# Kernel tuning notes

Hardware: AMD Instinct MI355X
Metric: run time of the kernel (lower is better)

## Reference

```python
import jax, jax.numpy as jnp
import numpy as np

B, C, H, W, A = 16, 4, 256, 256, 6
EPS = 1e-5


def _bn(z, s, b):
    # train-mode BatchNorm with batch size 1: reduce over (H, W) per channel, biased var
    m = z.mean((1, 2), keepdims=True)
    v = ((z - m) ** 2).mean((1, 2), keepdims=True)
    return (z - m) * jax.lax.rsqrt(v + EPS) * s[:, None, None] + b[:, None, None]


def _conv(z, w, pad, dil=1):
    # z: [C_in, H, W], w: [C_out, C_in, kh, kw]
    return jax.lax.conv_general_dilated(
        z[None], w, (1, 1), [(pad, pad), (pad, pad)],
        rhs_dilation=(dil, dil), dimension_numbers=("NCHW", "OIHW", "NCHW"))[0]


def _up2_axis(z, axis):
    # bilinear x2 with align_corners=True along one axis
    n = z.shape[axis]
    m = 2 * n
    pos = jnp.arange(m, dtype=jnp.float32) * ((n - 1) / (m - 1))
    i0 = jnp.floor(pos).astype(jnp.int32)
    i1 = jnp.minimum(i0 + 1, n - 1)
    f = pos - i0
    shape = [1] * z.ndim
    shape[axis] = m
    f = f.reshape(shape).astype(z.dtype)
    return jnp.take(z, i0, axis=axis) * (1 - f) + jnp.take(z, i1, axis=axis) * f


def _up2(z):
    return _up2_axis(_up2_axis(z, 1), 2)


def setup_inputs():
    key = jax.random.key(0)
    ks = jax.random.split(key, 16)
    inp = {}
    inp["x"] = jax.random.normal(ks[0], (B, C, H, W), jnp.float32)
    inp["action"] = jax.random.randint(ks[1], (B,), 0, A)
    # (out_features, init variance 2/(out_ch*k*k)) matching the torch init
    specs = [(16 * C * 25, 2.0 / (16 * 25)), (16 * 16 * 25, 2.0 / (16 * 25)),
             (32 * 16 * 25, 2.0 / (32 * 25)), (32 * 32 * 25, 2.0 / (32 * 25)),
             (64 * 32 * 25, 2.0 / (64 * 25)), (64 * 64 * 25, 2.0 / (64 * 25)),
             (4 * 64, 2.0 / 4.0)]
    for i, (od, var) in enumerate(specs):
        inp[f"w{i + 1}"] = jax.random.normal(ks[2 + i], (od, A), jnp.float32) * float(np.sqrt(var))
        inp[f"b{i + 1}"] = jnp.zeros((od,), jnp.float32)
    for i, ch in enumerate([C, 16, 16, 32, 32, 64, 64]):
        inp[f"bn{i}_s"] = jnp.ones((ch,), jnp.float32)
        inp[f"bn{i}_b"] = jnp.zeros((ch,), jnp.float32)
    return inp


def reference(x, action, w1, b1, w2, b2, w3, b3, w4, b4, w5, b5, w6, b6, w7, b7,
              bn0_s, bn0_b, bn1_s, bn1_b, bn2_s, bn2_b, bn3_s, bn3_b,
              bn4_s, bn4_b, bn5_s, bn5_b, bn6_s, bn6_b):
    onehot = jax.nn.one_hot(action, A, dtype=x.dtype)  # [B, A]

    def gen(w, b, shape):
        return (onehot @ w.T + b).reshape((x.shape[0],) + shape)

    y1 = gen(w1, b1, (16, C, 5, 5))
    y2 = gen(w2, b2, (16, 16, 5, 5))
    y3 = gen(w3, b3, (32, 16, 5, 5))
    y4 = gen(w4, b4, (32, 32, 5, 5))
    y5 = gen(w5, b5, (64, 32, 5, 5))
    y6 = gen(w6, b6, (64, 64, 5, 5))
    y7 = gen(w7, b7, (4, 64, 1, 1))

    def single(xi, k1, k2, k3, k4, k5, k6, k7):
        r = jax.nn.relu(_bn(_conv(_bn(xi, bn0_s, bn0_b), k1, 4, 2), bn1_s, bn1_b))
        r = _bn(_conv(r, k2, 2), bn2_s, bn2_b)
        c, h, w_ = r.shape  # avg_pool2d k=2 s=2
        r = r.reshape(c, h // 2, 2, w_ // 2, 2).mean((2, 4))
        r = jax.nn.relu(_bn(_conv(r, k3, 4, 2), bn3_s, bn3_b))
        r = _bn(_conv(r, k4, 2), bn4_s, bn4_b)
        r = jax.nn.relu(_bn(_conv(r, k5, 4, 2), bn5_s, bn5_b))
        r = _bn(_conv(r, k6, 2), bn6_s, bn6_b)
        r = _conv(r, k7, 0)  # 1x1 conv to `classes` channels
        return _up2(r)

    out = jax.vmap(single)(x, y1, y2, y3, y4, y5, y6, y7)
    return out + x
```

## Files before the change

### kernel.cpp

```cpp
#include <hip/hip_runtime.h>

#define NB 16
#define NA 6

typedef __attribute__((ext_vector_type(8))) short short8;
typedef __attribute__((ext_vector_type(4))) short short4_;
typedef __attribute__((ext_vector_type(4))) float f32x4;
typedef __attribute__((ext_vector_type(4))) unsigned uint4_;
typedef __attribute__((ext_vector_type(2))) unsigned uint2_;

__device__ __forceinline__ short tobf(float f) {
    unsigned u = __builtin_bit_cast(unsigned, f);
    u += 0x7FFF + ((u >> 16) & 1);
    return (short)(u >> 16);
}
__device__ __forceinline__ float frombf(short s) {
    unsigned u = ((unsigned)(unsigned short)s) << 16;
    return __builtin_bit_cast(float, u);
}
__device__ __forceinline__ unsigned cvtpk(float a, float b) {
    unsigned r;
    asm("v_cvt_pk_bf16_f32 %0, %1, %2" : "=v"(r) : "v"(a), "v"(b));
    return r;
}

template<int CIN, int COUT>
__device__ __forceinline__ void pack_one(const float* __restrict__ w, const float* __restrict__ bias,
                                         int a, int b, short* __restrict__ dst, int j) {
    constexpr int KTOT = 25 * CIN;
    constexpr int KPAD = (KTOT + 31) & ~31;
    if (j >= COUT * KPAD) return;
    int oc = j / KPAD, k = j - oc * KPAD;
    float v = 0.f;
    if (k < KTOT) {
        int pos = k / CIN, ci = k - pos * CIN;
        int ky = pos / 5, kx = pos - ky * 5;
        int od = ((oc * CIN + ci) * 5 + ky) * 5 + kx;
        v = w[(size_t)od * NA + a] + bias[od];
    }
    dst[((size_t)(b * (KPAD / 8) + (k >> 3)) * COUT + oc) * 8 + (k & 7)] = tobf(v);
}

__device__ __forceinline__ void pack_one8(const float* __restrict__ w, const float* __restrict__ bias,
                                          int a, int b, short* __restrict__ dst, int j) {
    if (j >= 16 * 224) return;
    int oc = j / 224, k = j - oc * 224;
    float v = 0.f;
    if (k < 200) {
        int pos = k >> 3, ci = k & 7;
        if (ci < 4) {
            int ky = pos / 5, kx = pos - ky * 5;
            int od = ((oc * 4 + ci) * 5 + ky) * 5 + kx;
            v = w[(size_t)od * NA + a] + bias[od];
        }
    }
    dst[((size_t)(b * 28 + (k >> 3)) * 16 + oc) * 8 + (k & 7)] = tobf(v);
}

__global__ void pack_all(const float* __restrict__ w2, const float* __restrict__ b2,
                         const float* __restrict__ w3, const float* __restrict__ b3,
                         const float* __restrict__ w4, const float* __restrict__ b4,
                         const float* __restrict__ w5, const float* __restrict__ b5,
                         const float* __restrict__ w6, const float* __restrict__ b6,
                         const float* __restrict__ w1, const float* __restrict__ b1,
                         const float* __restrict__ w7, const float* __restrict__ b7,
                         const int* __restrict__ action,
                         short* __restrict__ d2, short* __restrict__ d3, short* __restrict__ d4,
                         short* __restrict__ d5, short* __restrict__ d6,
                         short* __restrict__ d1, float* __restrict__ g7) {
    const int b = blockIdx.y;
    const int a = action[b];
    const int bx = blockIdx.x;
    const int t = threadIdx.x;
    if (bx < 26)       pack_one<16, 16>(w2, b2, a, b, d2, bx * 256 + t);
    else if (bx < 78)  pack_one<16, 32>(w3, b3, a, b, d3, (bx - 26) * 256 + t);
    else if (bx < 178) pack_one<32, 32>(w4, b4, a, b, d4, (bx - 78) * 256 + t);
    else if (bx < 378) pack_one<32, 64>(w5, b5, a, b, d5, (bx - 178) * 256 + t);
    else if (bx < 778) pack_one<64, 64>(w6, b6, a, b, d6, (bx - 378) * 256 + t);
    else if (bx < 792) pack_one8(w1, b1, a, b, d1, (bx - 778) * 256 + t);
    else               { g7[(size_t)b * 256 + t] = w7[(size_t)t * NA + a] + b7[t]; }
}

__global__ void stats0(const float* __restrict__ x, float* __restrict__ part0) {
    const int bc = blockIdx.y;
    const int b = bc >> 2, c = bc & 3;
    const float* p = x + ((size_t)bc << 16);
    const int base = blockIdx.x * 4096;
    float sum = 0.f, sq = 0.f;
    for (int i = threadIdx.x * 4; i < 4096; i += 1024) {
        float4 v = *(const float4*)(p + base + i);
        sum += (v.x + v.y) + (v.z + v.w);
        sq  += (v.x * v.x + v.y * v.y) + (v.z * v.z + v.w * v.w);
    }
#pragma unroll
    for (int off = 32; off > 0; off >>= 1) {
        sum += __shfl_down(sum, off);
        sq  += __shfl_down(sq, off);
    }
    __shared__ float ssum[4], ssq[4];
    int wv = threadIdx.x >> 6;
    if ((threadIdx.x & 63) == 0) { ssum[wv] = sum; ssq[wv] = sq; }
    __syncthreads();
    if (threadIdx.x == 0) {
        float S = ssum[0] + ssum[1] + ssum[2] + ssum[3];
        float Q = ssq[0] + ssq[1] + ssq[2] + ssq[3];
        atomicAdd(&part0[((size_t)b * 2 + 0) * 4 + c], S);
        atomicAdd(&part0[((size_t)b * 2 + 1) * 4 + c], Q);
    }
}

template<int C>
__device__ __forceinline__ void bn_fin8(const float* __restrict__ part,
                                        const float* __restrict__ sc,
                                        const float* __restrict__ bi,
                                        int b, int c0, float invN, f32x4* g, f32x4* e) {
#pragma unroll
    for (int h = 0; h < 2; ++h) {
        f32x4 Sv = *(const f32x4*)&part[((size_t)b * 2 + 0) * C + c0 + h * 4];
        f32x4 Qv = *(const f32x4*)&part[((size_t)b * 2 + 1) * C + c0 + h * 4];
        f32x4 scv = *(const f32x4*)&sc[c0 + h * 4];
        f32x4 biv = *(const f32x4*)&bi[c0 + h * 4];
#pragma unroll
        for (int j = 0; j < 4; ++j) {
            float m = Sv[j] * invN;
            float var = Qv[j] * invN - m * m;
            float gg = scv[j] * rsqrtf(var + 1e-5f);
            g[h][j] = gg;
            e[h][j] = biv[j] - m * gg;
        }
    }
}

__global__ void bnpool2(const short* __restrict__ in, short* __restrict__ out,
                        const float* __restrict__ part, const float* __restrict__ sc,
                        const float* __restrict__ bi) {
    const int b = blockIdx.y;
    const int c8 = threadIdx.x & 1;
    const int c0 = c8 * 8;
    f32x4 g[2], e[2];
    bn_fin8<16>(part, sc, bi, b, c0, 1.f / 65536.f, g, e);
    const size_t bin = (size_t)b * 65536 * 16;
    const size_t bout = (size_t)b * 16384 * 16;
    int total = 16384 * 2;
    int stride = gridDim.x * 256;
    for (int i = blockIdx.x * 256 + threadIdx.x; i < total; i += stride) {
        int opx = i >> 1;
        int ho = opx >> 7, wo = opx & 127;
        size_t p0 = bin + ((size_t)(ho * 2) * 256 + wo * 2) * 16 + c0;
        short8 v00 = *(const short8*)&in[p0];
        short8 v01 = *(const short8*)&in[p0 + 16];
        short8 v10 = *(const short8*)&in[p0 + 4096];
        short8 v11 = *(const short8*)&in[p0 + 4112];
        float f[8];
#pragma unroll
        for (int h = 0; h < 2; ++h)
#pragma unroll
            for (int j = 0; j < 4; ++j) {
                int k = h * 4 + j;
                float fv = (frombf(v00[k]) + frombf(v01[k]) + frombf(v10[k]) + frombf(v11[k])) * 0.25f;
                f[k] = fv * g[h][j] + e[h][j];
            }
        uint4_ vo = {cvtpk(f[0], f[1]), cvtpk(f[2], f[3]), cvtpk(f[4], f[5]), cvtpk(f[6], f[7])};
        *(uint4_*)&out[bout + (size_t)i * 8] = vo;
    }
}

template<int CIN, int COUT, int DIL, int WH, int PXB, int ROWS, int OCG, int WAVES, int APPLY, int INMODE = 0>
__global__ void __launch_bounds__(WAVES * 64) convmf8(const short* __restrict__ in,
                                                      const short* __restrict__ wpack,
                                                      short* __restrict__ outp,
                                                      float* __restrict__ partout,
                                                      const float* __restrict__ partin,
                                                      const float* __restrict__ psc,
                                                      const float* __restrict__ pbi,
                                                      float invN) {
    constexpr int PAD   = 2 * DIL;
    constexpr int XT    = PXB + 4 * DIL + 1;
    constexpr int LROWS = (DIL == 1) ? (ROWS + 4) : 5 * ROWS;
    constexpr int RSTR  = (DIL == 1) ? XT : 5 * XT;
    constexpr int KTOT  = 25 * CIN;
    constexpr int KPAD  = (KTOT + 31) & ~31;
    constexpr int NSTEP = KPAD / 32;
    constexpr int CINB  = CIN / 8;
    constexpr int S     = (CIN == 64) ? 0 : (CIN == 32) ? 1 : 2;
    constexpr int NTHR  = WAVES * 64;
    constexpr int PXG   = WAVES / OCG;
    constexpr int OT    = COUT / 16 / OCG;
    constexpr int PT    = ROWS * PXB / (16 * PXG);
    constexpr int LPXB  = (PXB == 32) ? 5 : (PXB == 64) ? 6 : 7;
    constexpr int LOGC  = (COUT == 64) ? 6 : (COUT == 32) ? 5 : 4;
    constexpr int CREAL = (INMODE == 1) ? 4 : CIN;
    constexpr int TBYTES = LROWS * XT * CIN * 2;
    static_assert(PXG * 2 * COUT * 4 <= TBYTES, "SP alias fits in T");
    static_assert(NSTEP >= 2, "pipeline depth");
    static_assert(PT * 16 * PXG == ROWS * PXB, "px cover");

    __shared__ __align__(16) char smem[TBYTES + 2 * 64 * 4];
    short* T  = (short*)smem;
    float* GA = (float*)(smem + TBYTES);
    float* BE = GA + 64;
    float* SP = (float*)smem;

    const int b   = blockIdx.z;
    const int y0  = blockIdx.y * ROWS;
    const int x0  = blockIdx.x * PXB;
    const int tid = threadIdx.x;

    if (APPLY) {
        if (tid < CREAL) {
            float S0 = partin[((size_t)b * 2 + 0) * CREAL + tid];
            float Q0 = partin[((size_t)b * 2 + 1) * CREAL + tid];
            float m = S0 * invN;
            float var = Q0 * invN - m * m;
            float g = psc[tid] * rsqrtf(var + 1e-5f);
            GA[tid] = g;
            BE[tid] = pbi[tid] - m * g;
        }
        __syncthreads();
    }

    if constexpr (INMODE == 1) {
        const float* xf = (const float*)in + ((size_t)b << 18);
        float g0 = GA[0], g1 = GA[1], g2 = GA[2], g3 = GA[3];
        float e0 = BE[0], e1 = BE[1], e2 = BE[2], e3 = BE[3];
        for (int idx = tid; idx < LROWS * XT; idx += NTHR) {
            int dyi = idx / XT, xl = idx - dyi * XT;
            int gy = (DIL == 1) ? (y0 + dyi - 2) : (y0 + dyi / 5 + 2 * (dyi % 5) - 4);
            int gx = x0 - PAD + xl;
            short8 v = {};
            if ((unsigned)gy < (unsigned)WH && (unsigned)gx < (unsigned)WH) {
                int o = (gy << 8) + gx;
                float f0 = xf[o] * g0 + e0;
                float f1 = xf[o + 65536] * g1 + e1;
                float f2 = xf[o + 131072] * g2 + e2;
                float f3 = xf[o + 196608] * g3 + e3;
                uint4_ uv = {cvtpk(f0, f1), cvtpk(f2, f3), 0u, 0u};
                v = __builtin_bit_cast(short8, uv);
            }
            *(short8*)&T[idx * CIN] = v;
        }
    } else {
        const short* inb = in + (size_t)b * WH * WH * CIN;
        for (int idx = tid; idx < LROWS * XT * CINB; idx += NTHR) {
            int dyi = idx / (XT * CINB);
            int rem = idx - dyi * (XT * CINB);
            int xl = rem / CINB, cic = rem - xl * CINB;
            int gy;
            if (DIL == 1) gy = y0 + dyi - 2;
            else          gy = y0 + dyi / 5 + 2 * (dyi % 5) - 4;
            int gx = x0 - PAD + xl;
            short8 v = {};
            if ((unsigned)gy < (unsigned)WH && (unsigned)gx < (unsigned)WH) {
                v = *(const short8*)&inb[((size_t)gy * WH + gx) * CIN + cic * 8];
                if (APPLY) {
                    float f[8];
#pragma unroll
                    for (int j = 0; j < 8; ++j) f[j] = frombf(v[j]);
                    f32x4 g0 = *(const f32x4*)&GA[cic * 8];
                    f32x4 g1 = *(const f32x4*)&GA[cic * 8 + 4];
                    f32x4 e0 = *(const f32x4*)&BE[cic * 8];
                    f32x4 e1 = *(const f32x4*)&BE[cic * 8 + 4];
#pragma unroll
                    for (int j = 0; j < 4; ++j) {
                        f[j]     = f[j]     * g0[j] + e0[j];
                        f[4 + j] = f[4 + j] * g1[j] + e1[j];
                        if (APPLY == 2) { f[j] = fmaxf(f[j], 0.f); f[4 + j] = fmaxf(f[4 + j], 0.f); }
                    }
                    uint4_ uv = {cvtpk(f[0], f[1]), cvtpk(f[2], f[3]),
                                 cvtpk(f[4], f[5]), cvtpk(f[6], f[7])};
                    v = __builtin_bit_cast(short8, uv);
                }
            }
            int r = dyi * XT + xl;
            int cs = (cic ^ ((r >> S) & (CINB - 1))) << 3;
            *(short8*)&T[r * CIN + cs] = v;
        }
    }
    __syncthreads();

    const int w = tid >> 6, lane = tid & 63;
    const int l15 = lane & 15, loct = lane >> 4;
    const int ocg = w & (OCG - 1);
    const int pxg = w / OCG;
    const int ocbase = ocg * OT * 16;
    const int pxbase = pxg * PT * 16;
    const int hsel = loct >> 1;
    (void)hsel;

    int bpt[PT];
#pragma unroll
    for (int pt = 0; pt < PT; ++pt) {
        int ppx = pxbase + pt * 16;
        bpt[pt] = (ppx >> LPXB) * RSTR + (ppx & (PXB - 1)) + l15;
    }

    const short* wl = wpack + (size_t)b * KPAD * COUT + ((size_t)loct * COUT + ocbase + l15) * 8;

    auto lA = [&](int s, short8* dst) {
        const short* ws = wl + (size_t)s * (4 * COUT * 8);
#pragma unroll
        for (int ot = 0; ot < OT; ++ot) dst[ot] = *(const short8*)&ws[ot * 128];
    };
    auto lB = [&](int s, short8* dst) {
        int Cs, cic;
        if constexpr (CIN == 64) {
            const int pos = s >> 1;
            Cs = (pos / 5) * XT + (pos % 5) * DIL;
            cic = (s & 1) * 4 + loct;
        } else if constexpr (CIN == 32) {
            Cs = (s / 5) * XT + (s % 5) * DIL;
            cic = loct;
        } else if constexpr (CIN == 8) {
            int pos = s * 4 + loct;
            if (pos > 24) pos = 24;
            Cs = (pos / 5) * XT + (pos % 5) * DIL;
            cic = 0;
        } else {
            const int p0 = (2 * s > 24) ? 24 : 2 * s;
            const int p1 = (2 * s + 1 > 24) ? 24 : 2 * s + 1;
            const int C0 = (p0 / 5) * XT + (p0 % 5) * DIL;
            const int C1 = (p1 / 5) * XT + (p1 % 5) * DIL;
            Cs = hsel ? C1 : C0;
            cic = loct & 1;
        }
#pragma unroll
        for (int pt = 0; pt < PT; ++pt) {
            int r = bpt[pt] + Cs;
            int chunk = cic ^ ((r >> S) & (CINB - 1));
            dst[pt] = *(const short8*)&T[r * CIN + (chunk << 3)];
        }
    };

    f32x4 acc[OT][PT] = {};
    short8 Acur[OT], Anx[OT], Bcur[PT];
    lA(0, Acur);
    lA(1, Anx);
    lB(0, Bcur);

    __builtin_amdgcn_s_setprio(1);
#pragma unroll
    for (int s = 0; s < NSTEP; ++s) {
        short8 An2[OT] = {}, Bn[PT] = {};
        if (s + 2 < NSTEP) lA(s + 2, An2);
        if (s + 1 < NSTEP) lB(s + 1, Bn);
#pragma unroll
        for (int ot = 0; ot < OT; ++ot)
#pragma unroll
            for (int pt = 0; pt < PT; ++pt)
                acc[ot][pt] = __builtin_amdgcn_mfma_f32_16x16x32_bf16(Acur[ot], Bcur[pt], acc[ot][pt], 0, 0, 0);
#pragma unroll
        for (int ot = 0; ot < OT; ++ot) { Acur[ot] = Anx[ot]; Anx[ot] = An2[ot]; }
#pragma unroll
        for (int pt = 0; pt < PT; ++pt) Bcur[pt] = Bn[pt];
    }
    __builtin_amdgcn_s_setprio(0);

#pragma unroll
    for (int ot = 0; ot < OT; ++ot)
#pragma unroll
        for (int pt = 0; pt < PT; ++pt) {
            int ppx = pxbase + pt * 16;
            int gpx = (y0 + (ppx >> LPXB)) * WH + x0 + (ppx & (PXB - 1)) + l15;
            int oc = ocbase + ot * 16 + (loct << 2);
            uint2_ st = {cvtpk(acc[ot][pt][0], acc[ot][pt][1]),
                         cvtpk(acc[ot][pt][2], acc[ot][pt][3])};
            *(uint2_*)&outp[((size_t)b * WH * WH + gpx) * COUT + oc] = st;
        }

    __syncthreads();

    float sv[OT][4], qv[OT][4];
#pragma unroll
    for (int ot = 0; ot < OT; ++ot)
#pragma unroll
        for (int j = 0; j < 4; ++j) {
            float sa = 0.f, qa = 0.f;
#pragma unroll
            for (int pt = 0; pt < PT; ++pt) { float v = acc[ot][pt][j]; sa += v; qa += v * v; }
#pragma unroll
            for (int m = 1; m <= 8; m <<= 1) { sa += __shfl_xor(sa, m); qa += __shfl_xor(qa, m); }
            sv[ot][j] = sa; qv[ot][j] = qa;
        }
    if (l15 == 0) {
#pragma unroll
        for (int ot = 0; ot < OT; ++ot)
#pragma unroll
            for (int j = 0; j < 4; ++j) {
                int c = ocbase + ot * 16 + (loct << 2) + j;
                SP[(pxg * 2 + 0) * COUT + c] = sv[ot][j];
                SP[(pxg * 2 + 1) * COUT + c] = qv[ot][j];
            }
    }
    __syncthreads();
    if (tid < 2 * COUT) {
        int m = tid >> LOGC, c = tid & (COUT - 1);
        float v = 0.f;
#pragma unroll
        for (int g = 0; g < PXG; ++g) v += SP[(g * 2 + m) * COUT + c];
        atomicAdd(&partout[((size_t)b * 2 + m) * COUT + c], v);
    }
}

__global__ void conv7k(const short* __restrict__ c6, const float* __restrict__ w7g,
                       const float* __restrict__ part, const float* __restrict__ sc,
                       const float* __restrict__ bi, float* __restrict__ c7) {
    __shared__ float wsm[256];
    __shared__ float GA[64], BE[64];
    const int b = blockIdx.y;
    const int t = threadIdx.x;
    wsm[t] = w7g[b * 256 + t];
    if (t < 64) {
        float S0 = part[((size_t)b * 2 + 0) * 64 + t];
        float Q0 = part[((size_t)b * 2 + 1) * 64 + t];
        float m = S0 * (1.f / 16384.f);
        float var = Q0 * (1.f / 16384.f) - m * m;
        float g = sc[t] * rsqrtf(var + 1e-5f);
        GA[t] = g;
        BE[t] = bi[t] - m * g;
    }
    __syncthreads();
    const int px = blockIdx.x * 64 + (t >> 2);
    const int q4 = t & 3;
    size_t base = ((size_t)b * 16384 + px) * 64 + q4 * 16;
    short8 s0 = *(const short8*)&c6[base];
    short8 s1 = *(const short8*)&c6[base + 8];
    f32x4 a = {0.f, 0.f, 0.f, 0.f};
#pragma unroll
    for (int ci = 0; ci < 8; ++ci) {
        float f0 = frombf(s0[ci]) * GA[q4 * 16 + ci] + BE[q4 * 16 + ci];
        float f1 = frombf(s1[ci]) * GA[q4 * 16 + 8 + ci] + BE[q4 * 16 + 8 + ci];
#pragma unroll
        for (int o = 0; o < 4; ++o) {
            a[o] = fmaf(f0, wsm[o * 64 + q4 * 16 + ci], a[o]);
            a[o] = fmaf(f1, wsm[o * 64 + q4 * 16 + 8 + ci], a[o]);
        }
    }
#pragma unroll
    for (int o = 0; o < 4; ++o) {
        a[o] += __shfl_xor(a[o], 1);
        a[o] += __shfl_xor(a[o], 2);
    }
    if (q4 == 0) *(f32x4*)&c7[((size_t)b * 16384 + px) * 4] = a;
}

__global__ void up2_add(const float* __restrict__ h, const float* __restrict__ xin,
                        float* __restrict__ outp, int total) {
    int stride = gridDim.x * blockDim.x;
    const float sc = 127.f / 255.f;
    for (int i = blockIdx.x * blockDim.x + threadIdx.x; i < total; i += stride) {
        int xo = i & 255, yo = (i >> 8) & 255, c = (i >> 16) & 3, b = i >> 18;
        float px = xo * sc, py = yo * sc;
        int x0 = (int)px, y0 = (int)py;
        float fx = px - x0, fy = py - y0;
        int x1 = min(x0 + 1, 127), y1 = min(y0 + 1, 127);
        const float* hb = h + ((size_t)b << 16);
        float v00 = hb[((y0 << 7) + x0) * 4 + c], v01 = hb[((y0 << 7) + x1) * 4 + c];
        float v10 = hb[((y1 << 7) + x0) * 4 + c], v11 = hb[((y1 << 7) + x1) * 4 + c];
        float vt = v00 + (v01 - v00) * fx;
        float vb = v10 + (v11 - v10) * fx;
        outp[i] = vt + (vb - vt) * fy + xin[i];
    }
}

extern "C" void kernel_launch(void* const* d_in, const int* in_sizes, int n_in,
                              void* d_out, int out_size, void* d_ws, size_t ws_size,
                              hipStream_t stream) {
    const float* x = (const float*)d_in[0];
    const int* action = (const int*)d_in[1];
    const float *W[7], *Bi[7], *bns[7], *bnb[7];
    for (int i = 0; i < 7; ++i) { W[i]   = (const float*)d_in[2 + 2 * i];
                                  Bi[i]  = (const float*)d_in[3 + 2 * i]; }
    for (int i = 0; i < 7; ++i) { bns[i] = (const float*)d_in[16 + 2 * i];
                                  bnb[i] = (const float*)d_in[17 + 2 * i]; }
    float* out = (float*)d_out;

    char* p = (char*)d_ws;
    auto carve = [&](size_t bytes) { char* r = p; p += (bytes + 255) & ~(size_t)255; return r; };
    float* w7g  = (float*)carve(256 * NB * 4);
    float* partAll = (float*)carve((size_t)NB * 2 * 228 * 4);
    float* p0 = partAll;
    float* p1 = p0 + NB * 2 * 4;
    float* p2 = p1 + NB * 2 * 16;
    float* p3 = p2 + NB * 2 * 16;
    float* p4 = p3 + NB * 2 * 32;
    float* p5 = p4 + NB * 2 * 32;
    float* p6 = p5 + NB * 2 * 64;
    short* wp1  = (short*)carve((size_t)224 * 16 * NB * 2);
    short* wp2  = (short*)carve((size_t)416 * 16 * NB * 2);
    short* wp3  = (short*)carve((size_t)416 * 32 * NB * 2);
    short* wp4  = (short*)carve((size_t)800 * 32 * NB * 2);
    short* wp5  = (short*)carve((size_t)800 * 64 * NB * 2);
    short* wp6  = (short*)carve((size_t)1600 * 64 * NB * 2);
    short* CB_A = (short*)carve((size_t)NB * 65536 * 16 * 2);
    short* CB_B = (short*)carve((size_t)NB * 65536 * 16 * 2);
    short* A0   = (short*)carve((size_t)NB * 65536 * 4 * 2);
    float* C7   = (float*)carve((size_t)NB * 16384 * 4 * 4);

    hipMemsetAsync(partAll, 0, (size_t)NB * 2 * 228 * 4, stream);

    pack_all<<<dim3(793, NB), 256, 0, stream>>>(
        W[1], Bi[1], W[2], Bi[2], W[3], Bi[3], W[4], Bi[4], W[5], Bi[5],
        W[0], Bi[0], W[6], Bi[6], action, wp2, wp3, wp4, wp5, wp6, wp1, w7g);

    stats0<<<dim3(16, 64), 256, 0, stream>>>(x, p0);

    convmf8<8, 16, 2, 256, 128, 2, 1, 8, 1, 1><<<dim3(2, 128, NB), 512, 0, stream>>>(
        (const short*)x, wp1, CB_A, p1, p0, bns[0], bnb[0], 1.f / 65536.f);

    convmf8<16, 16, 1, 256, 32, 16, 1, 8, 2><<<dim3(8, 16, NB), 512, 0, stream>>>(
        CB_A, wp2, CB_B, p2, p1, bns[1], bnb[1], 1.f / 65536.f);

    bnpool2<<<dim3(64, NB), 256, 0, stream>>>(CB_B, A0, p2, bns[2], bnb[2]);

    convmf8<16, 32, 2, 128, 128, 2, 1, 8, 0><<<dim3(1, 64, NB), 512, 0, stream>>>(
        A0, wp3, CB_A, p3, p2, bns[2], bnb[2], 1.f);

    convmf8<32, 32, 1, 128, 64, 8, 1, 8, 2><<<dim3(2, 16, NB), 512, 0, stream>>>(
        CB_A, wp4, CB_B, p4, p3, bns[3], bnb[3], 1.f / 16384.f);

    convmf8<32, 64, 2, 128, 128, 1, 2, 4, 1><<<dim3(1, 128, NB), 256, 0, stream>>>(
        CB_B, wp5, CB_A, p5, p4, bns[4], bnb[4], 1.f / 16384.f);

    convmf8<64, 64, 1, 128, 32, 8, 2, 8, 2><<<dim3(4, 16, NB), 512, 0, stream>>>(
        CB_A, wp6, CB_B, p6, p5, bns[5], bnb[5], 1.f / 16384.f);

    conv7k<<<dim3(256, NB), 256, 0, stream>>>(CB_B, w7g, p6, bns[6], bnb[6], C7);
    up2_add<<<4096, 256, 0, stream>>>(C7, x, out, 4194304);
}
```

Before: 278.4 us.

## Use 32x32x16 bf16 MFMA kernel for conv5 and conv6 layers

Adds a new conv kernel variant that uses 32x32x16 bf16 MFMA instructions with 16-float accumulators instead of the 16x16 tiles, and routes the two 64-output-channel layers through it. Each wave covers 32 output channels by 32 pixels per instruction, which halves the number of MFMA issues and fragment loads per unit of work. It also keeps a two-step-ahead prefetch of weights. The larger accumulator tiles raise register pressure and change the LDS read pattern, which may lower occupancy.

```diff
diff --git a/kernel.cpp b/kernel.cpp
--- a/kernel.cpp
+++ b/kernel.cpp
@@ -6,6 +6,7 @@
 typedef __attribute__((ext_vector_type(8))) short short8;
 typedef __attribute__((ext_vector_type(4))) short short4_;
 typedef __attribute__((ext_vector_type(4))) float f32x4;
+typedef __attribute__((ext_vector_type(16))) float f32x16;
 typedef __attribute__((ext_vector_type(4))) unsigned uint4_;
 typedef __attribute__((ext_vector_type(2))) unsigned uint2_;
 
@@ -401,6 +402,207 @@
     }
 }
 
+template<int CIN, int COUT, int DIL, int WH, int PXB, int ROWS, int WAVES, int APPLY>
+__global__ void __launch_bounds__(WAVES * 64) convmf9(const short* __restrict__ in,
+                                                      const short* __restrict__ wpack,
+                                                      short* __restrict__ outp,
+                                                      float* __restrict__ partout,
+                                                      const float* __restrict__ partin,
+                                                      const float* __restrict__ psc,
+                                                      const float* __restrict__ pbi,
+                                                      float invN) {
+    constexpr int PAD   = 2 * DIL;
+    constexpr int XT    = PXB + 4 * DIL + 1;
+    constexpr int LROWS = (DIL == 1) ? (ROWS + 4) : 5 * ROWS;
+    constexpr int RSTR  = (DIL == 1) ? XT : 5 * XT;
+    constexpr int KTOT  = 25 * CIN;
+    constexpr int KPAD  = (KTOT + 31) & ~31;
+    constexpr int NSTEP = KPAD / 16;
+    constexpr int CINB  = CIN / 8;
+    constexpr int S     = (CIN == 64) ? 0 : 1;
+    constexpr int NTHR  = WAVES * 64;
+    constexpr int PXG   = WAVES;
+    constexpr int OT    = COUT / 32;
+    constexpr int PT    = ROWS * PXB / (32 * PXG);
+    constexpr int LPXB  = (PXB == 32) ? 5 : (PXB == 64) ? 6 : 7;
+    constexpr int LOGC  = (COUT == 64) ? 6 : 5;
+    constexpr int TBYTES = LROWS * XT * CIN * 2;
+    static_assert(CIN == 32 || CIN == 64, "cin");
+    static_assert(PXG * 2 * COUT * 4 <= TBYTES, "SP alias fits in T");
+    static_assert(PT * 32 * PXG == ROWS * PXB, "px cover");
+
+    __shared__ __align__(16) char smem[TBYTES + 2 * 64 * 4];
+    short* T  = (short*)smem;
+    float* GA = (float*)(smem + TBYTES);
+    float* BE = GA + 64;
+    float* SP = (float*)smem;
+
+    const int b   = blockIdx.z;
+    const int y0  = blockIdx.y * ROWS;
+    const int x0  = blockIdx.x * PXB;
+    const int tid = threadIdx.x;
+
+    if (APPLY) {
+        if (tid < CIN) {
+            float S0 = partin[((size_t)b * 2 + 0) * CIN + tid];
+            float Q0 = partin[((size_t)b * 2 + 1) * CIN + tid];
+            float m = S0 * invN;
+            float var = Q0 * invN - m * m;
+            float g = psc[tid] * rsqrtf(var + 1e-5f);
+            GA[tid] = g;
+            BE[tid] = pbi[tid] - m * g;
+        }
+        __syncthreads();
+    }
+
+    const short* inb = in + (size_t)b * WH * WH * CIN;
+    for (int idx = tid; idx < LROWS * XT * CINB; idx += NTHR) {
+        int dyi = idx / (XT * CINB);
+        int rem = idx - dyi * (XT * CINB);
+        int xl = rem / CINB, cic = rem - xl * CINB;
+        int gy;
+        if (DIL == 1) gy = y0 + dyi - 2;
+        else          gy = y0 + dyi / 5 + 2 * (dyi % 5) - 4;
+        int gx = x0 - PAD + xl;
+        short8 v = {};
+        if ((unsigned)gy < (unsigned)WH && (unsigned)gx < (unsigned)WH) {
+            v = *(const short8*)&inb[((size_t)gy * WH + gx) * CIN + cic * 8];
+            if (APPLY) {
+                float f[8];
+#pragma unroll
+                for (int j = 0; j < 8; ++j) f[j] = frombf(v[j]);
+                f32x4 g0 = *(const f32x4*)&GA[cic * 8];
+                f32x4 g1 = *(const f32x4*)&GA[cic * 8 + 4];
+                f32x4 e0 = *(const f32x4*)&BE[cic * 8];
+                f32x4 e1 = *(const f32x4*)&BE[cic * 8 + 4];
+#pragma unroll
+                for (int j = 0; j < 4; ++j) {
+                    f[j]     = f[j]     * g0[j] + e0[j];
+                    f[4 + j] = f[4 + j] * g1[j] + e1[j];
+                    if (APPLY == 2) { f[j] = fmaxf(f[j], 0.f); f[4 + j] = fmaxf(f[4 + j], 0.f); }
+                }
+                uint4_ uv = {cvtpk(f[0], f[1]), cvtpk(f[2], f[3]),
+                             cvtpk(f[4], f[5]), cvtpk(f[6], f[7])};
+                v = __builtin_bit_cast(short8, uv);
+            }
+        }
+        int r = dyi * XT + xl;
+        int cs = (cic ^ ((r >> S) & (CINB - 1))) << 3;
+        *(short8*)&T[r * CIN + cs] = v;
+    }
+    __syncthreads();
+
+    const int w = tid >> 6, lane = tid & 63;
+    const int l31 = lane & 31, kh = lane >> 5;
+    const int pxg = w;
+    const int pxbase = pxg * PT * 32;
+
+    int bpt[PT];
+#pragma unroll
+    for (int pt = 0; pt < PT; ++pt) {
+        int ppx = pxbase + pt * 32;
+        bpt[pt] = (ppx >> LPXB) * RSTR + (ppx & (PXB - 1)) + l31;
+    }
+
+    const short* wl = wpack + (size_t)b * KPAD * COUT + ((size_t)kh * COUT + l31) * 8;
+
+    auto lA = [&](int s, short8* dst) {
+        const short* ws = wl + (size_t)s * (2 * COUT * 8);
+#pragma unroll
+        for (int ot = 0; ot < OT; ++ot) dst[ot] = *(const short8*)&ws[ot * 256];
+    };
+    auto lB = [&](int s, short8* dst) {
+        int Cs, cic;
+        if constexpr (CIN == 64) {
+            const int pos = s >> 2;
+            Cs = (pos / 5) * XT + (pos % 5) * DIL;
+            cic = (s & 3) * 2 + kh;
+        } else {
+            const int pos = s >> 1;
+            Cs = (pos / 5) * XT + (pos % 5) * DIL;
+            cic = (s & 1) * 2 + kh;
+        }
+#pragma unroll
+        for (int pt = 0; pt < PT; ++pt) {
+            int r = bpt[pt] + Cs;
+            int chunk = cic ^ ((r >> S) & (CINB - 1));
+            dst[pt] = *(const short8*)&T[r * CIN + (chunk << 3)];
+        }
+    };
+
+    f32x16 acc[OT][PT] = {};
+    short8 Acur[OT], Anx[OT], Bcur[PT];
+    lA(0, Acur);
+    lA(1, Anx);
+    lB(0, Bcur);
+
+    __builtin_amdgcn_s_setprio(1);
+#pragma unroll
+    for (int s = 0; s < NSTEP; ++s) {
+        short8 An2[OT] = {}, Bn[PT] = {};
+        if (s + 2 < NSTEP) lA(s + 2, An2);
+        if (s + 1 < NSTEP) lB(s + 1, Bn);
+#pragma unroll
+        for (int ot = 0; ot < OT; ++ot)
+#pragma unroll
+            for (int pt = 0; pt < PT; ++pt)
+                acc[ot][pt] = __builtin_amdgcn_mfma_f32_32x32x16_bf16(Acur[ot], Bcur[pt], acc[ot][pt], 0, 0, 0);
+#pragma unroll
+        for (int ot = 0; ot < OT; ++ot) { Acur[ot] = Anx[ot]; Anx[ot] = An2[ot]; }
+#pragma unroll
+        for (int pt = 0; pt < PT; ++pt) Bcur[pt] = Bn[pt];
+    }
+    __builtin_amdgcn_s_setprio(0);
+
+#pragma unroll
+    for (int ot = 0; ot < OT; ++ot)
+#pragma unroll
+        for (int pt = 0; pt < PT; ++pt) {
+            int ppx = pxbase + pt * 32;
+            int gpx = (y0 + (ppx >> LPXB)) * WH + x0 + (ppx & (PXB - 1)) + l31;
+#pragma unroll
+            for (int q = 0; q < 4; ++q) {
+                int oc = ot * 32 + q * 8 + kh * 4;
+                uint2_ st = {cvtpk(acc[ot][pt][q * 4], acc[ot][pt][q * 4 + 1]),
+                             cvtpk(acc[ot][pt][q * 4 + 2], acc[ot][pt][q * 4 + 3])};
+                *(uint2_*)&outp[((size_t)b * WH * WH + gpx) * COUT + oc] = st;
+            }
+        }
+
+    __syncthreads();
+
+    float sv[OT][16], qv[OT][16];
+#pragma unroll
+    for (int ot = 0; ot < OT; ++ot)
+#pragma unroll
+        for (int r = 0; r < 16; ++r) {
+            float sa = 0.f, qa = 0.f;
+#pragma unroll
+            for (int pt = 0; pt < PT; ++pt) { float v = acc[ot][pt][r]; sa += v; qa += v * v; }
+#pragma unroll
+            for (int m = 1; m <= 16; m <<= 1) { sa += __shfl_xor(sa, m); qa += __shfl_xor(qa, m); }
+            sv[ot][r] = sa; qv[ot][r] = qa;
+        }
+    if (l31 == 0) {
+#pragma unroll
+        for (int ot = 0; ot < OT; ++ot)
+#pragma unroll
+            for (int r = 0; r < 16; ++r) {
+                int c = ot * 32 + (r >> 2) * 8 + kh * 4 + (r & 3);
+                SP[(pxg * 2 + 0) * COUT + c] = sv[ot][r];
+                SP[(pxg * 2 + 1) * COUT + c] = qv[ot][r];
+            }
+    }
+    __syncthreads();
+    if (tid < 2 * COUT) {
+        int m = tid >> LOGC, c = tid & (COUT - 1);
+        float v = 0.f;
+#pragma unroll
+        for (int g = 0; g < PXG; ++g) v += SP[(g * 2 + m) * COUT + c];
+        atomicAdd(&partout[((size_t)b * 2 + m) * COUT + c], v);
+    }
+}
+
 __global__ void conv7k(const short* __restrict__ c6, const float* __restrict__ w7g,
                        const float* __restrict__ part, const float* __restrict__ sc,
                        const float* __restrict__ bi, float* __restrict__ c7) {
@@ -518,10 +720,10 @@
     convmf8<32, 32, 1, 128, 64, 8, 1, 8, 2><<<dim3(2, 16, NB), 512, 0, stream>>>(
         CB_A, wp4, CB_B, p4, p3, bns[3], bnb[3], 1.f / 16384.f);
 
-    convmf8<32, 64, 2, 128, 128, 1, 2, 4, 1><<<dim3(1, 128, NB), 256, 0, stream>>>(
+    convmf9<32, 64, 2, 128, 128, 1, 4, 1><<<dim3(1, 128, NB), 256, 0, stream>>>(
         CB_B, wp5, CB_A, p5, p4, bns[4], bnb[4], 1.f / 16384.f);
 
-    convmf8<64, 64, 1, 128, 32, 8, 2, 8, 2><<<dim3(4, 16, NB), 512, 0, stream>>>(
+    convmf9<64, 64, 1, 128, 32, 8, 8, 2><<<dim3(4, 16, NB), 512, 0, stream>>>(
         CB_A, wp6, CB_B, p6, p5, bns[5], bnb[5], 1.f / 16384.f);
 
     conv7k<<<dim3(256, NB), 256, 0, stream>>>(CB_B, w7g, p6, bns[6], bnb[6], C7);
```

New measurement: 359.0 us. 28.9% more time.
